# Kernel tuning notes

Measured on AMD Instinct MI355X. Metric: run time of the kernel, lower is better.

The kernel has to match this reference:

```python
import jax, jax.numpy as jnp
import numpy as np
import math

D_SINGLE, D_PAIR, H, PQ, PV = 384, 128, 12, 4, 8
DH = D_SINGLE // H
OUT_DIM = H * DH + H * PV * 4 + H * D_PAIR


def setup_inputs() -> dict:
    key = jax.random.key(0)
    ks = jax.random.split(key, 24)
    B, L = 1, 512
    inp = {
        'single': jax.random.normal(ks[0], (B, L, D_SINGLE), jnp.float32),
        'pair': jax.random.normal(ks[1], (B, L, L, D_PAIR), jnp.float32),
        'rot_mats': jax.random.normal(ks[2], (B, L, 3, 3), jnp.float32),
        'trans': jax.random.normal(ks[3], (B, L, 3), jnp.float32),
        'mask': jnp.ones((B, L), jnp.float32),
        'ln_w': jnp.ones((D_SINGLE,), jnp.float32),
        'ln_b': jnp.zeros((D_SINGLE,), jnp.float32),
        'Wq': jax.random.normal(ks[4], (D_SINGLE, H * DH), jnp.float32) * 0.02,
        'bq': jnp.zeros((H * DH,), jnp.float32),
        'Wk': jax.random.normal(ks[5], (D_SINGLE, H * DH), jnp.float32) * 0.02,
        'bk': jnp.zeros((H * DH,), jnp.float32),
        'Wv': jax.random.normal(ks[6], (D_SINGLE, H * DH), jnp.float32) * 0.02,
        'bv': jnp.zeros((H * DH,), jnp.float32),
        'Wqp': jax.random.normal(ks[7], (D_SINGLE, H * PQ * 3), jnp.float32) * 0.02,
        'bqp': jnp.zeros((H * PQ * 3,), jnp.float32),
        'Wkp': jax.random.normal(ks[8], (D_SINGLE, H * PQ * 3), jnp.float32) * 0.02,
        'bkp': jnp.zeros((H * PQ * 3,), jnp.float32),
        'Wvp': jax.random.normal(ks[9], (D_SINGLE, H * PV * 3), jnp.float32) * 0.02,
        'bvp': jnp.zeros((H * PV * 3,), jnp.float32),
        'Wpb': jax.random.normal(ks[10], (D_PAIR, H), jnp.float32) * 0.02,
        'bpb': jnp.zeros((H,), jnp.float32),
        'Wo': jax.random.normal(ks[11], (OUT_DIM, D_SINGLE), jnp.float32) * 0.02,
        'bo': jnp.zeros((D_SINGLE,), jnp.float32),
        'w_c': jnp.asarray(1.0 / math.sqrt(3.0), jnp.float32),
        'w_l': jnp.asarray(1.0 / 3.0, jnp.float32),
        'gamma_h': jnp.ones((H,), jnp.float32),
    }
    return inp


def _layer_norm(x, w, b, eps=1e-5):
    mu = jnp.mean(x, axis=-1, keepdims=True)
    var = jnp.mean((x - mu) ** 2, axis=-1, keepdims=True)
    return (x - mu) * jax.lax.rsqrt(var + eps) * w + b


def reference(single, pair, rot_mats, trans, mask, ln_w, ln_b, Wq, bq, Wk, bk, Wv, bv,
              Wqp, bqp, Wkp, bkp, Wvp, bvp, Wpb, bpb, Wo, bo, w_c, w_l, gamma_h):
    B, L, _ = single.shape
    sn = _layer_norm(single, ln_w, ln_b)
    q = (sn @ Wq + bq).reshape(B, L, H, DH)
    k = (sn @ Wk + bk).reshape(B, L, H, DH)
    v = (sn @ Wv + bv).reshape(B, L, H, DH)
    qp = (sn @ Wqp + bqp).reshape(B, L, H, PQ, 3)
    kp = (sn @ Wkp + bkp).reshape(B, L, H, PQ, 3)
    vp = (sn @ Wvp + bvp).reshape(B, L, H, PV, 3)

    t = trans[:, :, None, None, :]  # [B,L,1,1,3]
    qg = jnp.einsum('blij,blhpj->blhpi', rot_mats, qp) + t
    kg = jnp.einsum('blij,blhpj->blhpi', rot_mats, kp) + t
    vg = jnp.einsum('blij,blhpj->blhpi', rot_mats, vp) + t

    # sequence logits [B,H,L,L]
    seq_logits = jnp.einsum('bihd,bjhd->bhij', q, k) * w_c / math.sqrt(DH)

    # geometric logits: pairwise point distances [B,H,L,L]
    q_pts = jnp.transpose(qg, (0, 2, 1, 3, 4))  # [B,H,L,PQ,3]
    k_pts = jnp.transpose(kg, (0, 2, 1, 3, 4))
    diff = q_pts[:, :, :, None] - k_pts[:, :, None]  # [B,H,L,L,PQ,3]
    dist_sq = jnp.sum(diff ** 2, axis=-1)            # [B,H,L,L,PQ]
    geo_logits = -0.5 * jnp.sum(dist_sq, axis=-1) * gamma_h[None, :, None, None] * w_l

    pair_bias = jnp.transpose(pair @ Wpb + bpb, (0, 3, 1, 2))  # [B,H,L,L]
    logits = seq_logits + geo_logits + pair_bias

    mask_2d = (mask[:, :, None] * mask[:, None, :])[:, None]  # [B,1,L,L]
    logits = jnp.where(mask_2d > 0, logits, jnp.float32(-1e9))
    attn = jax.nn.softmax(logits, axis=-1)  # [B,H,L,L]

    # sequence aggregation -> [B,L,H,DH]
    seq_out = jnp.einsum('bhij,bjhd->bihd', attn, v).reshape(B, L, H * DH)

    # point aggregation -> local frame features
    pts_out = jnp.einsum('bhij,bjhpd->bihpd', attn, vg)  # [B,L,H,PV,3]
    pts_local = jnp.einsum('blji,blhpj->blhpi', rot_mats, pts_out - t)
    pts_norm = jnp.linalg.norm(pts_local, axis=-1, keepdims=True)
    pts_feat = jnp.concatenate([pts_norm, pts_local], axis=-1).reshape(B, L, H * PV * 4)

    # pair aggregation -> [B,L,H*D_PAIR]
    pair_out = jnp.einsum('bhij,bijd->bihd', attn, pair).reshape(B, L, H * D_PAIR)

    combined = jnp.concatenate([seq_out, pts_feat, pair_out], axis=-1)
    return combined @ Wo + bo
```

## Files before the change

### kernel.cpp

```cpp
#include <hip/hip_runtime.h>
#include <math.h>

#define LQ    512
#define DS    384
#define DPAIR 128
#define NH    12
#define NPP   1792
#define TJC   64
#define NC    8

typedef unsigned short u16;
typedef unsigned int   u32;
typedef __attribute__((ext_vector_type(8))) short bf16x8;
typedef __attribute__((ext_vector_type(4))) float f32x4;

__device__ inline u16 bf16_rne(float x) {
  u32 u = __float_as_uint(x);
  u32 r = (u + 0x7FFFu + ((u >> 16) & 1u)) >> 16;
  return (u16)r;
}
__device__ inline void split_bf16(float x, u16& h, u16& l) {
  u16 hb = bf16_rne(x);
  float hf = __uint_as_float(((u32)hb) << 16);
  h = hb;
  l = bf16_rne(x - hf);
}

__device__ inline void async_copy16(const float* g, float* l) {
  auto gp = (const __attribute__((address_space(1))) float*)(g);
  auto lp = (__attribute__((address_space(3))) float*)(l);
  __builtin_amdgcn_global_load_lds(gp, lp, 16, 0, 0);
}

__global__ __launch_bounds__(256) void k_prep(
    const float* __restrict__ Wq, const float* __restrict__ Wk,
    const float* __restrict__ Wv, const float* __restrict__ Wqp,
    const float* __restrict__ Wkp, const float* __restrict__ Wvp,
    const float* __restrict__ bq, const float* __restrict__ bk,
    const float* __restrict__ bv, const float* __restrict__ bqp,
    const float* __restrict__ bkp, const float* __restrict__ bvp,
    const float* __restrict__ Wpb, const float* __restrict__ Wo,
    const float* __restrict__ xs, const float* __restrict__ ln_w,
    const float* __restrict__ ln_b,
    u16* __restrict__ Wth, u16* __restrict__ Wtl,
    float* __restrict__ bcat, float* __restrict__ WpbT,
    u16* __restrict__ WoTh, u16* __restrict__ WoTl,
    u16* __restrict__ snh, u16* __restrict__ snl) {
  __shared__ u16 sh_hi[64][66], sh_lo[64][66];
  int blk = blockIdx.x, t = threadIdx.x;
  if (blk < 168) {
    int kb = blk / 28, cb = blk % 28;
    int k0 = kb * 64, c0 = cb * 64;
    for (int e = t; e < 4096; e += 256) {
      int rr = e >> 6, cc = e & 63;
      int k = k0 + rr, c = c0 + cc;
      float v = 0.f;
      if (c < 384)       v = Wq[k*384 + c];
      else if (c < 768)  v = Wk[k*384 + c-384];
      else if (c < 1152) v = Wv[k*384 + c-768];
      else if (c < 1296) v = Wqp[k*144 + c-1152];
      else if (c < 1440) v = Wkp[k*144 + c-1296];
      else if (c < 1728) v = Wvp[k*288 + c-1440];
      u16 h_, l_; split_bf16(v, h_, l_);
      sh_hi[rr][cc] = h_; sh_lo[rr][cc] = l_;
    }
    __syncthreads();
    for (int e = t; e < 4096; e += 256) {
      int cc = e >> 6, kk = e & 63;
      Wth[(size_t)(c0+cc)*DS + k0 + kk] = sh_hi[kk][cc];
      Wtl[(size_t)(c0+cc)*DS + k0 + kk] = sh_lo[kk][cc];
    }
  } else if (blk == 168) {
    for (int e = t; e < NPP + NH*DPAIR; e += 256) {
      if (e < NPP) {
        int c = e;
        float v = 0.f;
        if (c < 384)       v = bq[c];
        else if (c < 768)  v = bk[c-384];
        else if (c < 1152) v = bv[c-768];
        else if (c < 1296) v = bqp[c-1152];
        else if (c < 1440) v = bkp[c-1296];
        else if (c < 1728) v = bvp[c-1440];
        bcat[c] = v;
      } else {
        int e2 = e - NPP;
        int k = e2 / NH, h = e2 % NH;
        WpbT[h*DPAIR + k] = Wpb[e2];
      }
    }
  } else if (blk < 385) {
    int idx = blk - 169;
    int kt = idx % 36, nt = idx / 36;
    int k0 = kt * 64, n0 = nt * 64;
    for (int e = t; e < 4096; e += 256) {
      int rr = e >> 6, cc = e & 63;
      float v = Wo[(size_t)(k0+rr)*384 + n0 + cc];
      u16 h_, l_; split_bf16(v, h_, l_);
      sh_hi[rr][cc] = h_; sh_lo[rr][cc] = l_;
    }
    __syncthreads();
    for (int e = t; e < 4096; e += 256) {
      int cc = e >> 6, kk = e & 63;
      WoTh[(size_t)(n0+cc)*2304 + k0 + kk] = sh_hi[kk][cc];
      WoTl[(size_t)(n0+cc)*2304 + k0 + kk] = sh_lo[kk][cc];
    }
  } else {
    int i = blk - 385;
    float* red = (float*)&sh_hi[0][0];
    float a0 = xs[i*DS + t];
    float a1 = (t < 128) ? xs[i*DS + 256 + t] : 0.f;
    red[t] = a0 + a1; __syncthreads();
    for (int s = 128; s > 0; s >>= 1) { if (t < s) red[t] += red[t+s]; __syncthreads(); }
    float mu = red[0] * (1.f/384.f);
    __syncthreads();
    float d0 = a0 - mu, d1 = (t < 128) ? (a1 - mu) : 0.f;
    red[t] = d0*d0 + d1*d1; __syncthreads();
    for (int s = 128; s > 0; s >>= 1) { if (t < s) red[t] += red[t+s]; __syncthreads(); }
    float rstd = rsqrtf(red[0] * (1.f/384.f) + 1e-5f);
    u16 h_, l_;
    float y0 = d0*rstd*ln_w[t] + ln_b[t];
    split_bf16(y0, h_, l_); snh[i*DS + t] = h_; snl[i*DS + t] = l_;
    if (t < 128) {
      float y1 = d1*rstd*ln_w[256+t] + ln_b[256+t];
      split_bf16(y1, h_, l_); snh[i*DS + 256 + t] = h_; snl[i*DS + 256 + t] = l_;
    }
  }
}

__global__ __launch_bounds__(256) void k_gemm_mfma(
    const u16* __restrict__ Ah, const u16* __restrict__ Al,
    const u16* __restrict__ Bth, const u16* __restrict__ Btl,
    const float* __restrict__ bias, float* __restrict__ C,
    float* __restrict__ Cpart, int M, int N, int K) {
  int t = threadIdx.x;
  int lane = t & 63, wave = t >> 6;
  int wr = wave >> 1, wc = wave & 1;
  int i0 = blockIdx.y * 64 + wr * 32;
  int j0 = blockIdx.x * 64 + wc * 32;
  int KS = gridDim.z;
  int kper = K / KS;
  size_t kbeg = (size_t)blockIdx.z * kper;
  int lr = lane & 15, lk = (lane >> 4) << 3;

  const u16* a0h = Ah  + (size_t)(i0 + lr) * K + kbeg + lk;
  const u16* a1h = a0h + (size_t)16 * K;
  const u16* a0l = Al  + (size_t)(i0 + lr) * K + kbeg + lk;
  const u16* a1l = a0l + (size_t)16 * K;
  const u16* b0h = Bth + (size_t)(j0 + lr) * K + kbeg + lk;
  const u16* b1h = b0h + (size_t)16 * K;
  const u16* b0l = Btl + (size_t)(j0 + lr) * K + kbeg + lk;
  const u16* b1l = b0l + (size_t)16 * K;

  f32x4 c00 = {0.f,0.f,0.f,0.f}, c01 = c00, c10 = c00, c11 = c00;
  for (int k = 0; k < kper; k += 32) {
    bf16x8 A0h = *(const bf16x8*)(a0h + k);
    bf16x8 A1h = *(const bf16x8*)(a1h + k);
    bf16x8 B0h = *(const bf16x8*)(b0h + k);
    bf16x8 B1h = *(const bf16x8*)(b1h + k);
    bf16x8 A0l = *(const bf16x8*)(a0l + k);
    bf16x8 A1l = *(const bf16x8*)(a1l + k);
    bf16x8 B0l = *(const bf16x8*)(b0l + k);
    bf16x8 B1l = *(const bf16x8*)(b1l + k);
    c00 = __builtin_amdgcn_mfma_f32_16x16x32_bf16(A0h, B0h, c00, 0, 0, 0);
    c01 = __builtin_amdgcn_mfma_f32_16x16x32_bf16(A0h, B1h, c01, 0, 0, 0);
    c10 = __builtin_amdgcn_mfma_f32_16x16x32_bf16(A1h, B0h, c10, 0, 0, 0);
    c11 = __builtin_amdgcn_mfma_f32_16x16x32_bf16(A1h, B1h, c11, 0, 0, 0);
    c00 = __builtin_amdgcn_mfma_f32_16x16x32_bf16(A0h, B0l, c00, 0, 0, 0);
    c01 = __builtin_amdgcn_mfma_f32_16x16x32_bf16(A0h, B1l, c01, 0, 0, 0);
    c10 = __builtin_amdgcn_mfma_f32_16x16x32_bf16(A1h, B0l, c10, 0, 0, 0);
    c11 = __builtin_amdgcn_mfma_f32_16x16x32_bf16(A1h, B1l, c11, 0, 0, 0);
    c00 = __builtin_amdgcn_mfma_f32_16x16x32_bf16(A0l, B0h, c00, 0, 0, 0);
    c01 = __builtin_amdgcn_mfma_f32_16x16x32_bf16(A0l, B1h, c01, 0, 0, 0);
    c10 = __builtin_amdgcn_mfma_f32_16x16x32_bf16(A1l, B0h, c10, 0, 0, 0);
    c11 = __builtin_amdgcn_mfma_f32_16x16x32_bf16(A1l, B1h, c11, 0, 0, 0);
  }

  int orow = (lane >> 4) << 2;
  int col0 = j0 + lr, col1 = j0 + 16 + lr;
  if (KS == 1) {
    float bb0 = bias[col0], bb1 = bias[col1];
    #pragma unroll
    for (int r = 0; r < 4; r++) {
      int row0 = i0 + orow + r, row1 = row0 + 16;
      C[(size_t)row0*N + col0] = c00[r] + bb0;
      C[(size_t)row0*N + col1] = c01[r] + bb1;
      C[(size_t)row1*N + col0] = c10[r] + bb0;
      C[(size_t)row1*N + col1] = c11[r] + bb1;
    }
  } else {
    float* dst = Cpart + (size_t)blockIdx.z * M * N;
    #pragma unroll
    for (int r = 0; r < 4; r++) {
      int row0 = i0 + orow + r, row1 = row0 + 16;
      dst[(size_t)row0*N + col0] = c00[r];
      dst[(size_t)row0*N + col1] = c01[r];
      dst[(size_t)row1*N + col0] = c10[r];
      dst[(size_t)row1*N + col1] = c11[r];
    }
  }
}

__global__ void k_reduce_bias(const float* __restrict__ part, const float* __restrict__ bias,
                              float* __restrict__ out, int MN, int N, int KS) {
  int e = blockIdx.x * 256 + threadIdx.x;
  if (e >= MN) return;
  float s = bias[e % N];
  for (int z = 0; z < KS; z++) s += part[(size_t)z*MN + e];
  out[e] = s;
}

__global__ __launch_bounds__(256) void k_feat_logits(
    const float* __restrict__ C1, const float* __restrict__ rot,
    const float* __restrict__ trans, const float* __restrict__ gamma,
    const float* __restrict__ w_c, const float* __restrict__ w_l,
    float* __restrict__ S) {
  __shared__ u16 Ash[64][72], Asl[64][72], Bsh[64][72], Bsl[64][72];
  int h = blockIdx.z;
  int i0 = blockIdx.y * 64, j0 = blockIdx.x * 64;
  int t = threadIdx.x;

  if (t < 128) {
    int row = t & 63, side = t >> 6;
    int gi = (side ? j0 : i0) + row;
    float R[9], tr[3];
    #pragma unroll
    for (int r = 0; r < 9; r++) R[r] = rot[(size_t)gi*9 + r];
    #pragma unroll
    for (int r = 0; r < 3; r++) tr[r] = trans[(size_t)gi*3 + r];
    float sc = w_c[0] * rsqrtf(32.f);
    float gp = gamma[h] * w_l[0];
    u16 (*Fh)[72] = side ? Bsh : Ash;
    u16 (*Fl)[72] = side ? Bsl : Asl;
    const float* qk = C1 + (size_t)gi*NPP + (side ? 384 : 0) + h*32;
    u16 h_, l_;
    #pragma unroll 8
    for (int d = 0; d < 32; d++) {
      float v = side ? qk[d] : sc*qk[d];
      split_bf16(v, h_, l_); Fh[row][d] = h_; Fl[row][d] = l_;
    }
    const float* pp = C1 + (size_t)gi*NPP + (side ? 1296 : 1152) + h*12;
    float ss = 0.f;
    #pragma unroll
    for (int p = 0; p < 4; p++) {
      float x = pp[p*3], y = pp[p*3+1], z = pp[p*3+2];
      #pragma unroll
      for (int r = 0; r < 3; r++) {
        float g = fmaf(R[r*3],x, fmaf(R[r*3+1],y, fmaf(R[r*3+2],z, tr[r])));
        float v = side ? g : gp*g;
        split_bf16(v, h_, l_); Fh[row][32+p*3+r] = h_; Fl[row][32+p*3+r] = l_;
        ss = fmaf(g,g,ss);
      }
    }
    float c44 = side ? 1.f : -0.5f*gp*ss;
    float c45 = side ? -0.5f*gp*ss : 1.f;
    split_bf16(c44, h_, l_); Fh[row][44] = h_; Fl[row][44] = l_;
    split_bf16(c45, h_, l_); Fh[row][45] = h_; Fl[row][45] = l_;
    #pragma unroll
    for (int d = 46; d < 64; d++) { Fh[row][d] = 0; Fl[row][d] = 0; }
  }
  __syncthreads();

  int lane = t & 63, wave = t >> 6, wr = wave >> 1, wc = wave & 1;
  int lr = lane & 15, lk = (lane >> 4) << 3;
  f32x4 c00 = {0.f,0.f,0.f,0.f}, c01 = c00, c10 = c00, c11 = c00;
  #pragma unroll
  for (int ks = 0; ks < 64; ks += 32) {
    bf16x8 A0h = *(const bf16x8*)&Ash[wr*32 + lr][ks + lk];
    bf16x8 A1h = *(const bf16x8*)&Ash[wr*32 + 16 + lr][ks + lk];
    bf16x8 B0h = *(const bf16x8*)&Bsh[wc*32 + lr][ks + lk];
    bf16x8 B1h = *(const bf16x8*)&Bsh[wc*32 + 16 + lr][ks + lk];
    bf16x8 A0l = *(const bf16x8*)&Asl[wr*32 + lr][ks + lk];
    bf16x8 A1l = *(const bf16x8*)&Asl[wr*32 + 16 + lr][ks + lk];
    bf16x8 B0l = *(const bf16x8*)&Bsl[wc*32 + lr][ks + lk];
    bf16x8 B1l = *(const bf16x8*)&Bsl[wc*32 + 16 + lr][ks + lk];
    c00 = __builtin_amdgcn_mfma_f32_16x16x32_bf16(A0h, B0h, c00, 0, 0, 0);
    c01 = __builtin_amdgcn_mfma_f32_16x16x32_bf16(A0h, B1h, c01, 0, 0, 0);
    c10 = __builtin_amdgcn_mfma_f32_16x16x32_bf16(A1h, B0h, c10, 0, 0, 0);
    c11 = __builtin_amdgcn_mfma_f32_16x16x32_bf16(A1h, B1h, c11, 0, 0, 0);
    c00 = __builtin_amdgcn_mfma_f32_16x16x32_bf16(A0h, B0l, c00, 0, 0, 0);
    c01 = __builtin_amdgcn_mfma_f32_16x16x32_bf16(A0h, B1l, c01, 0, 0, 0);
    c10 = __builtin_amdgcn_mfma_f32_16x16x32_bf16(A1h, B0l, c10, 0, 0, 0);
    c11 = __builtin_amdgcn_mfma_f32_16x16x32_bf16(A1h, B1l, c11, 0, 0, 0);
    c00 = __builtin_amdgcn_mfma_f32_16x16x32_bf16(A0l, B0h, c00, 0, 0, 0);
    c01 = __builtin_amdgcn_mfma_f32_16x16x32_bf16(A0l, B1h, c01, 0, 0, 0);
    c10 = __builtin_amdgcn_mfma_f32_16x16x32_bf16(A1l, B0h, c10, 0, 0, 0);
    c11 = __builtin_amdgcn_mfma_f32_16x16x32_bf16(A1l, B1h, c11, 0, 0, 0);
  }

  int orow = (lane >> 4) << 2;
  int col0 = j0 + wc*32 + lr, col1 = col0 + 16;
  int rbase = i0 + wr*32 + orow;
  #pragma unroll
  for (int r = 0; r < 4; r++) {
    S[((size_t)h*LQ + rbase + r)*LQ + col0]      = c00[r];
    S[((size_t)h*LQ + rbase + r)*LQ + col1]      = c01[r];
    S[((size_t)h*LQ + rbase + 16 + r)*LQ + col0] = c10[r];
    S[((size_t)h*LQ + rbase + 16 + r)*LQ + col1] = c11[r];
  }
}

__global__ __launch_bounds__(256) void k_vt(
    const float* __restrict__ C1, const float* __restrict__ rot,
    const float* __restrict__ trans,
    u16* __restrict__ Vth, u16* __restrict__ Vtl) {
  int h = blockIdx.x;
  int i = blockIdx.y * 256 + threadIdx.x;
  float R[9], tr[3];
  #pragma unroll
  for (int r = 0; r < 9; r++) R[r] = rot[(size_t)i*9 + r];
  #pragma unroll
  for (int r = 0; r < 3; r++) tr[r] = trans[(size_t)i*3 + r];
  const float* vrow = C1 + (size_t)i*NPP + 768 + h*32;
  const float* prow = C1 + (size_t)i*NPP + 1440 + h*24;
  u16 h_, l_;
  #pragma unroll 8
  for (int n = 0; n < 32; n++) {
    split_bf16(vrow[n], h_, l_);
    Vth[((size_t)h*64 + n)*LQ + i] = h_;
    Vtl[((size_t)h*64 + n)*LQ + i] = l_;
  }
  #pragma unroll
  for (int p = 0; p < 8; p++) {
    float x = prow[p*3], y = prow[p*3+1], z = prow[p*3+2];
    #pragma unroll
    for (int r = 0; r < 3; r++) {
      float g = fmaf(R[r*3],x, fmaf(R[r*3+1],y, fmaf(R[r*3+2],z, tr[r])));
      split_bf16(g, h_, l_);
      Vth[((size_t)h*64 + 32 + p*3 + r)*LQ + i] = h_;
      Vtl[((size_t)h*64 + 32 + p*3 + r)*LQ + i] = l_;
    }
  }
  #pragma unroll
  for (int n = 56; n < 64; n++) {
    Vth[((size_t)h*64 + n)*LQ + i] = 0;
    Vtl[((size_t)h*64 + n)*LQ + i] = 0;
  }
}

__global__ __launch_bounds__(256) void k_pair(
    const float* __restrict__ pair, const float* __restrict__ WpbT,
    const float* __restrict__ bpb, const float* __restrict__ mask,
    float* S, float* __restrict__ scs_g,
    u16* __restrict__ combh, u16* __restrict__ combl) {
  __shared__ float tile[2][TJC*DPAIR];
  __shared__ float wt[NH*TJC];
  __shared__ float msc[NC][NH], ssc[NC][NH];
  __shared__ float rfac[NH], dinv[NH];
  int i = blockIdx.x, t = threadIdx.x;
  int lane = t & 63, wave = t >> 6;
  int j = lane;
  int h0 = wave * 3;
  int dg = t & 31, strip = t >> 5, jb = strip*8;

  const float* prow = pair + (size_t)i*LQ*DPAIR;
  float b0 = bpb[h0], b1 = bpb[h0+1], b2 = bpb[h0+2];
  float mi = mask[i];
  const float* w0p = WpbT + (size_t)(h0+0)*DPAIR;
  const float* w1p = WpbT + (size_t)(h0+1)*DPAIR;
  const float* w2p = WpbT + (size_t)(h0+2)*DPAIR;

  float4 acc[NH];
  #pragma unroll
  for (int h = 0; h < NH; h++) acc[h] = make_float4(0.f,0.f,0.f,0.f);
  float mrun[3] = {-3.0e38f, -3.0e38f, -3.0e38f};

  auto dma = [&](int c, int buf) {
    #pragma unroll
    for (int u = 0; u < 8; u++) {
      int seg = wave*8 + u;
      int F = seg*64 + lane;
      int row = F >> 5, k4s = F & 31;
      int k4 = k4s ^ (row & 7);
      const float* src = prow + (size_t)(c*TJC + row)*DPAIR + k4*4;
      async_copy16(src, &tile[buf][seg*256]);
    }
  };

  dma(0, 0);
  asm volatile("s_waitcnt vmcnt(0)" ::: "memory");
  __syncthreads();
  int cur = 0;

  for (int c = 0; c < NC; c++) {
    if (c < NC-1) dma(c+1, cur^1);
    int j0 = c*TJC;
    float l0 = S[((size_t)(h0+0)*LQ + i)*LQ + j0 + j] + b0;
    float l1 = S[((size_t)(h0+1)*LQ + i)*LQ + j0 + j] + b1;
    float l2 = S[((size_t)(h0+2)*LQ + i)*LQ + j0 + j] + b2;
    {
      float a0 = 0.f, a1 = 0.f, a2 = 0.f;
      #pragma unroll 8
      for (int kk = 0; kk < 32; kk++) {
        float4 pv = *(const float4*)&tile[cur][(j*32 + (kk ^ (j & 7)))*4];
        float4 w0 = *(const float4*)(w0p + kk*4);
        float4 w1 = *(const float4*)(w1p + kk*4);
        float4 w2 = *(const float4*)(w2p + kk*4);
        a0 = fmaf(pv.x,w0.x, fmaf(pv.y,w0.y, fmaf(pv.z,w0.z, fmaf(pv.w,w0.w, a0))));
        a1 = fmaf(pv.x,w1.x, fmaf(pv.y,w1.y, fmaf(pv.z,w1.z, fmaf(pv.w,w1.w, a1))));
        a2 = fmaf(pv.x,w2.x, fmaf(pv.y,w2.y, fmaf(pv.z,w2.z, fmaf(pv.w,w2.w, a2))));
      }
      l0 += a0; l1 += a1; l2 += a2;
      bool dead = (mi * mask[j0 + j] <= 0.f);
      if (dead) { l0 = -1e9f; l1 = -1e9f; l2 = -1e9f; }
    }
    #pragma unroll
    for (int q = 0; q < 3; q++) {
      float lv = (q==0) ? l0 : (q==1) ? l1 : l2;
      float m = lv;
      #pragma unroll
      for (int o = 32; o > 0; o >>= 1) m = fmaxf(m, __shfl_xor(m, o, 64));
      float w = __expf(lv - m);
      float sm = w;
      #pragma unroll
      for (int o = 32; o > 0; o >>= 1) sm += __shfl_xor(sm, o, 64);
      float mnew = fmaxf(mrun[q], m);
      float f  = __expf(m - mnew);
      float rf = __expf(mrun[q] - mnew);
      mrun[q] = mnew;
      wt[(h0+q)*TJC + j] = w * f;
      S[((size_t)(h0+q)*LQ + i)*LQ + j0 + j] = w;
      if (j == 0) { msc[c][h0+q] = m; ssc[c][h0+q] = sm; rfac[h0+q] = rf; }
    }
    __syncthreads();
    {
      float4 pv[8];
      #pragma unroll
      for (int q = 0; q < 8; q++) {
        int row = jb + q;
        pv[q] = *(const float4*)&tile[cur][(row*32 + (dg ^ (row & 7)))*4];
      }
      #pragma unroll
      for (int h = 0; h < NH; h++) {
        float rf = rfac[h];
        float4 w0 = *(const float4*)&wt[h*TJC + jb];
        float4 w1 = *(const float4*)&wt[h*TJC + jb + 4];
        float wq[8] = {w0.x,w0.y,w0.z,w0.w,w1.x,w1.y,w1.z,w1.w};
        float4 a = acc[h];
        a.x *= rf; a.y *= rf; a.z *= rf; a.w *= rf;
        #pragma unroll
        for (int q = 0; q < 8; q++) {
          a.x = fmaf(wq[q], pv[q].x, a.x);
          a.y = fmaf(wq[q], pv[q].y, a.y);
          a.z = fmaf(wq[q], pv[q].z, a.z);
          a.w = fmaf(wq[q], pv[q].w, a.w);
        }
        acc[h] = a;
      }
    }
    asm volatile("s_waitcnt vmcnt(0)" ::: "memory");
    __syncthreads();
    cur ^= 1;
  }

  if (j == 0) {
    #pragma unroll
    for (int q = 0; q < 3; q++) {
      float M = mrun[q];
      float den = 0.f;
      #pragma unroll
      for (int c = 0; c < NC; c++) den += ssc[c][h0+q] * __expf(msc[c][h0+q] - M);
      float inv = 1.f / den;
      dinv[h0+q] = inv;
      #pragma unroll
      for (int c = 0; c < NC; c++)
        scs_g[((size_t)i*NH + h0+q)*NC + c] = __expf(msc[c][h0+q] - M) * inv;
    }
  }

  float4* red4 = (float4*)&tile[0][0];
  float4 tot[2];
  tot[0] = make_float4(0.f,0.f,0.f,0.f);
  tot[1] = make_float4(0.f,0.f,0.f,0.f);
  #pragma unroll
  for (int half = 0; half < 2; half++) {
    if ((strip >> 2) == half) {
      #pragma unroll
      for (int h = 0; h < NH; h++)
        red4[(((strip & 3)*NH) + h)*32 + dg] = acc[h];
    }
    __syncthreads();
    for (int e = t, u = 0; e < NH*32; e += 256, u++) {
      int rh = e >> 5, rd = e & 31;
      #pragma unroll
      for (int s4 = 0; s4 < 4; s4++) {
        float4 v = red4[((s4*NH) + rh)*32 + rd];
        tot[u].x += v.x; tot[u].y += v.y; tot[u].z += v.z; tot[u].w += v.w;
      }
    }
    __syncthreads();
  }
  for (int e = t, u = 0; e < NH*32; e += 256, u++) {
    int rh = e >> 5, rd = e & 31;
    float inv = dinv[rh];
    size_t dst = (size_t)i*2304 + 768 + rh*DPAIR + rd*4;
    u16 h_, l_;
    split_bf16(tot[u].x * inv, h_, l_); combh[dst+0] = h_; combl[dst+0] = l_;
    split_bf16(tot[u].y * inv, h_, l_); combh[dst+1] = h_; combl[dst+1] = l_;
    split_bf16(tot[u].z * inv, h_, l_); combh[dst+2] = h_; combl[dst+2] = l_;
    split_bf16(tot[u].w * inv, h_, l_); combh[dst+3] = h_; combl[dst+3] = l_;
  }
}

__global__ __launch_bounds__(256) void k_attn_mfma(
    const float* __restrict__ S, const float* __restrict__ scs_g,
    const u16* __restrict__ Vth, const u16* __restrict__ Vtl,
    float* __restrict__ psum) {
  int t = threadIdx.x;
  int lane = t & 63, wave = t >> 6;
  int wr = wave >> 1, wc = wave & 1;
  int z = blockIdx.x;
  int i0 = blockIdx.y * 64 + wr * 32;
  int h = blockIdx.z;
  int n0 = wc * 32;
  int lr = lane & 15, lk = (lane >> 4) << 3;

  const float* a0p = S + ((size_t)h*LQ + i0 + lr)*LQ + z*128 + lk;
  const float* a1p = a0p + (size_t)16*LQ;
  const float* s0p = scs_g + ((size_t)(i0 + lr)*NH + h)*NC + z*2;
  const float* s1p = scs_g + ((size_t)(i0 + 16 + lr)*NH + h)*NC + z*2;
  const u16* b0h = Vth + ((size_t)h*64 + n0 + lr)*LQ + z*128 + lk;
  const u16* b1h = b0h + (size_t)16*LQ;
  const u16* b0l = Vtl + ((size_t)h*64 + n0 + lr)*LQ + z*128 + lk;
  const u16* b1l = b0l + (size_t)16*LQ;

  f32x4 c00 = {0.f,0.f,0.f,0.f}, c01 = c00, c10 = c00, c11 = c00;
  #pragma unroll
  for (int k = 0; k < 128; k += 32) {
    int cc = (k >= 64) ? 1 : 0;
    float sc0 = s0p[cc], sc1 = s1p[cc];
    float4 av00 = *(const float4*)(a0p + k);
    float4 av01 = *(const float4*)(a0p + k + 4);
    float4 av10 = *(const float4*)(a1p + k);
    float4 av11 = *(const float4*)(a1p + k + 4);
    float a0v[8] = {av00.x,av00.y,av00.z,av00.w,av01.x,av01.y,av01.z,av01.w};
    float a1v[8] = {av10.x,av10.y,av10.z,av10.w,av11.x,av11.y,av11.z,av11.w};
    bf16x8 A0h = {}, A0l = {}, A1h = {}, A1l = {};
    #pragma unroll
    for (int e = 0; e < 8; e++) {
      u16 hh, ll;
      split_bf16(a0v[e]*sc0, hh, ll);
      A0h[e] = (short)hh; A0l[e] = (short)ll;
      split_bf16(a1v[e]*sc1, hh, ll);
      A1h[e] = (short)hh; A1l[e] = (short)ll;
    }
    bf16x8 B0h = *(const bf16x8*)(b0h + k);
    bf16x8 B1h = *(const bf16x8*)(b1h + k);
    bf16x8 B0l = *(const bf16x8*)(b0l + k);
    bf16x8 B1l = *(const bf16x8*)(b1l + k);
    c00 = __builtin_amdgcn_mfma_f32_16x16x32_bf16(A0h, B0h, c00, 0, 0, 0);
    c01 = __builtin_amdgcn_mfma_f32_16x16x32_bf16(A0h, B1h, c01, 0, 0, 0);
    c10 = __builtin_amdgcn_mfma_f32_16x16x32_bf16(A1h, B0h, c10, 0, 0, 0);
    c11 = __builtin_amdgcn_mfma_f32_16x16x32_bf16(A1h, B1h, c11, 0, 0, 0);
    c00 = __builtin_amdgcn_mfma_f32_16x16x32_bf16(A0h, B0l, c00, 0, 0, 0);
    c01 = __builtin_amdgcn_mfma_f32_16x16x32_bf16(A0h, B1l, c01, 0, 0, 0);
    c10 = __builtin_amdgcn_mfma_f32_16x16x32_bf16(A1h, B0l, c10, 0, 0, 0);
    c11 = __builtin_amdgcn_mfma_f32_16x16x32_bf16(A1h, B1l, c11, 0, 0, 0);
    c00 = __builtin_amdgcn_mfma_f32_16x16x32_bf16(A0l, B0h, c00, 0, 0, 0);
    c01 = __builtin_amdgcn_mfma_f32_16x16x32_bf16(A0l, B1h, c01, 0, 0, 0);
    c10 = __builtin_amdgcn_mfma_f32_16x16x32_bf16(A1l, B0h, c10, 0, 0, 0);
    c11 = __builtin_amdgcn_mfma_f32_16x16x32_bf16(A1l, B1h, c11, 0, 0, 0);
  }

  int orow = (lane >> 4) << 2;
  int col0 = n0 + lr, col1 = n0 + 16 + lr;
  #pragma unroll
  for (int r = 0; r < 4; r++) {
    int row0 = i0 + orow + r, row1 = row0 + 16;
    psum[(((size_t)z*LQ + row0)*NH + h)*64 + col0] = c00[r];
    psum[(((size_t)z*LQ + row0)*NH + h)*64 + col1] = c01[r];
    psum[(((size_t)z*LQ + row1)*NH + h)*64 + col0] = c10[r];
    psum[(((size_t)z*LQ + row1)*NH + h)*64 + col1] = c11[r];
  }
}

__global__ void k_avpts(const float* __restrict__ psum, const float* __restrict__ rot,
                        const float* __restrict__ trans,
                        u16* __restrict__ combh, u16* __restrict__ combl) {
  int idx = blockIdx.x * 256 + threadIdx.x;
  if (idx >= LQ*NH*40) return;
  int w = idx % 40; int ih = idx / 40; int h = ih % NH; int i = ih / NH;
  size_t base = ((size_t)i*NH + h)*64;
  u16 h_, l_;
  if (w < 32) {
    float s = 0.f;
    for (int z = 0; z < 4; z++) s += psum[(size_t)z*LQ*NH*64 + base + w];
    split_bf16(s, h_, l_);
    combh[(size_t)i*2304 + h*32 + w] = h_;
    combl[(size_t)i*2304 + h*32 + w] = l_;
  } else {
    int p = w - 32;
    float g[3];
    #pragma unroll
    for (int r = 0; r < 3; r++) {
      int n = 32 + p*3 + r;
      float s = 0.f;
      for (int z = 0; z < 4; z++) s += psum[(size_t)z*LQ*NH*64 + base + n];
      g[r] = s;
    }
    const float* R = rot + (size_t)i*9;
    const float* tr = trans + (size_t)i*3;
    float x = g[0]-tr[0], y = g[1]-tr[1], z = g[2]-tr[2];
    float lx = fmaf(R[0],x, fmaf(R[3],y, R[6]*z));
    float ly = fmaf(R[1],x, fmaf(R[4],y, R[7]*z));
    float lz = fmaf(R[2],x, fmaf(R[5],y, R[8]*z));
    float nrm = sqrtf(fmaf(lx,lx, fmaf(ly,ly, lz*lz)));
    size_t dst = (size_t)i*2304 + 384 + (h*8 + p)*4;
    split_bf16(nrm, h_, l_); combh[dst+0] = h_; combl[dst+0] = l_;
    split_bf16(lx,  h_, l_); combh[dst+1] = h_; combl[dst+1] = l_;
    split_bf16(ly,  h_, l_); combh[dst+2] = h_; combl[dst+2] = l_;
    split_bf16(lz,  h_, l_); combh[dst+3] = h_; combl[dst+3] = l_;
  }
}

extern "C" void kernel_launch(void* const* d_in, const int* in_sizes, int n_in,
                              void* d_out, int out_size, void* d_ws, size_t ws_size,
                              hipStream_t stream) {
  const float* single = (const float*)d_in[0];
  const float* pair   = (const float*)d_in[1];
  const float* rot    = (const float*)d_in[2];
  const float* trans  = (const float*)d_in[3];
  const float* mask   = (const float*)d_in[4];
  const float* ln_w   = (const float*)d_in[5];
  const float* ln_b   = (const float*)d_in[6];
  const float* Wq     = (const float*)d_in[7];
  const float* bq     = (const float*)d_in[8];
  const float* Wk     = (const float*)d_in[9];
  const float* bk     = (const float*)d_in[10];
  const float* Wv     = (const float*)d_in[11];
  const float* bv     = (const float*)d_in[12];
  const float* Wqp    = (const float*)d_in[13];
  const float* bqp    = (const float*)d_in[14];
  const float* Wkp    = (const float*)d_in[15];
  const float* bkp    = (const float*)d_in[16];
  const float* Wvp    = (const float*)d_in[17];
  const float* bvp    = (const float*)d_in[18];
  const float* Wpb    = (const float*)d_in[19];
  const float* bpb    = (const float*)d_in[20];
  const float* Wo     = (const float*)d_in[21];
  const float* bo     = (const float*)d_in[22];
  const float* w_c    = (const float*)d_in[23];
  const float* w_l    = (const float*)d_in[24];
  const float* gamma  = (const float*)d_in[25];
  float* out = (float*)d_out;

  float* p = (float*)d_ws;
  auto alloc = [&](size_t n) { float* r = p; p += n; return r; };
  u16* WcatTh = (u16*)alloc((size_t)NPP*DS/2);
  u16* WcatTl = (u16*)alloc((size_t)NPP*DS/2);
  u16* snh    = (u16*)alloc((size_t)LQ*DS/2);
  u16* snl    = (u16*)alloc((size_t)LQ*DS/2);
  u16* WoTh   = (u16*)alloc((size_t)DS*2304/2);
  u16* WoTl   = (u16*)alloc((size_t)DS*2304/2);
  u16* combh  = (u16*)alloc((size_t)LQ*2304/2);
  u16* combl  = (u16*)alloc((size_t)LQ*2304/2);
  u16* Vth    = (u16*)alloc((size_t)NH*64*LQ/2);
  u16* Vtl    = (u16*)alloc((size_t)NH*64*LQ/2);
  float* bcat    = alloc(NPP);
  float* WpbT    = alloc((size_t)NH*DPAIR);
  float* C1      = alloc((size_t)LQ*NPP);
  float* S       = alloc((size_t)NH*LQ*LQ);
  float* scs_g   = alloc((size_t)LQ*NH*NC);
  float* psum    = alloc((size_t)4*LQ*NH*64);
  float* outpart = alloc((size_t)8*LQ*DS);

  k_prep<<<dim3(897), 256, 0, stream>>>(
      Wq, Wk, Wv, Wqp, Wkp, Wvp, bq, bk, bv, bqp, bkp, bvp, Wpb, Wo,
      single, ln_w, ln_b, WcatTh, WcatTl, bcat, WpbT, WoTh, WoTl, snh, snl);
  k_gemm_mfma<<<dim3(NPP/64, LQ/64, 1), 256, 0, stream>>>(
      snh, snl, WcatTh, WcatTl, bcat, C1, nullptr, LQ, NPP, DS);
  k_feat_logits<<<dim3(LQ/64, LQ/64, NH), 256, 0, stream>>>(
      C1, rot, trans, gamma, w_c, w_l, S);
  k_vt<<<dim3(NH, LQ/256), 256, 0, stream>>>(C1, rot, trans, Vth, Vtl);
  k_pair<<<dim3(LQ), 256, 0, stream>>>(
      pair, WpbT, bpb, mask, S, scs_g, combh, combl);
  k_attn_mfma<<<dim3(4, LQ/64, NH), 256, 0, stream>>>(
      S, scs_g, Vth, Vtl, psum);
  k_avpts<<<dim3((LQ*NH*40 + 255)/256), 256, 0, stream>>>(
      psum, rot, trans, combh, combl);
  k_gemm_mfma<<<dim3(DS/64, LQ/64, 8), 256, 0, stream>>>(
      combh, combl, WoTh, WoTl, nullptr, nullptr, outpart, LQ, DS, 2304);
  k_reduce_bias<<<dim3((LQ*DS + 255)/256), 256, 0, stream>>>(outpart, bo, out, LQ*DS, DS, 8);
}
```

Measured before the change: 376.1 us.

## Split pair-attention kernel into per-chunk blocks with separate softmax combine kernel

The per-row pair kernel, which looped serially over 8 key chunks with async double-buffered loads and an online softmax, is replaced by a grid of (row, chunk) blocks. Each block computes local softmax stats and a partial pair aggregation into a global workspace, and a new small kernel merges the chunk maxima and sums and writes the normalized pair output. This gives 8x more blocks for the pass over the large pair tensor and drops the serial dependency, at the cost of a partial-sum round trip through global memory, an extra launch, and plain (non-async) tile loads.

```diff
diff --git a/kernel.cpp b/kernel.cpp
--- a/kernel.cpp
+++ b/kernel.cpp
@@ -24,12 +24,6 @@
   float hf = __uint_as_float(((u32)hb) << 16);
   h = hb;
   l = bf16_rne(x - hf);
-}
-
-__device__ inline void async_copy16(const float* g, float* l) {
-  auto gp = (const __attribute__((address_space(1))) float*)(g);
-  auto lp = (__attribute__((address_space(3))) float*)(l);
-  __builtin_amdgcn_global_load_lds(gp, lp, 16, 0, 0);
 }
 
 __global__ __launch_bounds__(256) void k_prep(
@@ -337,137 +331,94 @@
   }
 }
 
-__global__ __launch_bounds__(256) void k_pair(
+__global__ __launch_bounds__(256, 2) void k_pair_chunk(
     const float* __restrict__ pair, const float* __restrict__ WpbT,
     const float* __restrict__ bpb, const float* __restrict__ mask,
-    float* S, float* __restrict__ scs_g,
-    u16* __restrict__ combh, u16* __restrict__ combl) {
-  __shared__ float tile[2][TJC*DPAIR];
+    float* __restrict__ S, float* __restrict__ pairpart, float* __restrict__ msum) {
+  __shared__ float tile[TJC*133];
   __shared__ float wt[NH*TJC];
-  __shared__ float msc[NC][NH], ssc[NC][NH];
-  __shared__ float rfac[NH], dinv[NH];
-  int i = blockIdx.x, t = threadIdx.x;
-  int lane = t & 63, wave = t >> 6;
-  int j = lane;
-  int h0 = wave * 3;
+  int i = blockIdx.x, c = blockIdx.y, t = threadIdx.x;
+  int j0 = c*TJC;
+
+  const float4* src = (const float4*)(pair + ((size_t)i*LQ + j0)*DPAIR);
+  #pragma unroll
+  for (int u = 0; u < 8; u++) {
+    int e = t + u*256; int row = e >> 5, c4 = e & 31;
+    *(float4*)&tile[row*133 + c4*4] = src[e];
+  }
+
+  int j = t & 63;
+  int hg = __builtin_amdgcn_readfirstlane(t >> 6);
+  int h0 = hg*3;
+  float l[3];
+  #pragma unroll
+  for (int q = 0; q < 3; q++)
+    l[q] = S[((size_t)(h0+q)*LQ + i)*LQ + j0 + j] + bpb[h0+q];
+  bool dead = (mask[i] * mask[j0 + j] <= 0.f);
+  __syncthreads();
+
+  {
+    const float* w0p = WpbT + (size_t)(h0+0)*DPAIR;
+    const float* w1p = WpbT + (size_t)(h0+1)*DPAIR;
+    const float* w2p = WpbT + (size_t)(h0+2)*DPAIR;
+    float a0 = 0.f, a1 = 0.f, a2 = 0.f;
+    #pragma unroll 8
+    for (int k = 0; k < DPAIR; k += 4) {
+      float4 pv = *(const float4*)&tile[j*133 + k];
+      float4 w0 = *(const float4*)(w0p + k);
+      float4 w1 = *(const float4*)(w1p + k);
+      float4 w2 = *(const float4*)(w2p + k);
+      a0 = fmaf(pv.x,w0.x, fmaf(pv.y,w0.y, fmaf(pv.z,w0.z, fmaf(pv.w,w0.w, a0))));
+      a1 = fmaf(pv.x,w1.x, fmaf(pv.y,w1.y, fmaf(pv.z,w1.z, fmaf(pv.w,w1.w, a1))));
+      a2 = fmaf(pv.x,w2.x, fmaf(pv.y,w2.y, fmaf(pv.z,w2.z, fmaf(pv.w,w2.w, a2))));
+    }
+    l[0] += a0; l[1] += a1; l[2] += a2;
+    if (dead) { l[0] = -1e9f; l[1] = -1e9f; l[2] = -1e9f; }
+  }
+
+  #pragma unroll
+  for (int q = 0; q < 3; q++) {
+    float m = l[q];
+    #pragma unroll
+    for (int o = 32; o > 0; o >>= 1) m = fmaxf(m, __shfl_xor(m, o, 64));
+    float w = __expf(l[q] - m);
+    float sm = w;
+    #pragma unroll
+    for (int o = 32; o > 0; o >>= 1) sm += __shfl_xor(sm, o, 64);
+    wt[(h0+q)*TJC + j] = w;
+    S[((size_t)(h0+q)*LQ + i)*LQ + j0 + j] = w;
+    if (j == 0) {
+      float* dst = msum + (((size_t)i*NC + c)*NH + h0 + q)*2;
+      dst[0] = m; dst[1] = sm;
+    }
+  }
+  __syncthreads();
+
   int dg = t & 31, strip = t >> 5, jb = strip*8;
-
-  const float* prow = pair + (size_t)i*LQ*DPAIR;
-  float b0 = bpb[h0], b1 = bpb[h0+1], b2 = bpb[h0+2];
-  float mi = mask[i];
-  const float* w0p = WpbT + (size_t)(h0+0)*DPAIR;
-  const float* w1p = WpbT + (size_t)(h0+1)*DPAIR;
-  const float* w2p = WpbT + (size_t)(h0+2)*DPAIR;
-
+  float4 pv[8];
+  #pragma unroll
+  for (int q = 0; q < 8; q++) pv[q] = *(const float4*)&tile[(jb+q)*133 + dg*4];
   float4 acc[NH];
   #pragma unroll
   for (int h = 0; h < NH; h++) acc[h] = make_float4(0.f,0.f,0.f,0.f);
-  float mrun[3] = {-3.0e38f, -3.0e38f, -3.0e38f};
-
-  auto dma = [&](int c, int buf) {
-    #pragma unroll
-    for (int u = 0; u < 8; u++) {
-      int seg = wave*8 + u;
-      int F = seg*64 + lane;
-      int row = F >> 5, k4s = F & 31;
-      int k4 = k4s ^ (row & 7);
-      const float* src = prow + (size_t)(c*TJC + row)*DPAIR + k4*4;
-      async_copy16(src, &tile[buf][seg*256]);
-    }
-  };
-
-  dma(0, 0);
-  asm volatile("s_waitcnt vmcnt(0)" ::: "memory");
+  #pragma unroll
+  for (int h = 0; h < NH; h++) {
+    float4 w0 = *(const float4*)&wt[h*TJC + jb];
+    float4 w1 = *(const float4*)&wt[h*TJC + jb + 4];
+    float wq[8] = {w0.x,w0.y,w0.z,w0.w,w1.x,w1.y,w1.z,w1.w};
+    float4 a = acc[h];
+    #pragma unroll
+    for (int q = 0; q < 8; q++) {
+      a.x = fmaf(wq[q], pv[q].x, a.x);
+      a.y = fmaf(wq[q], pv[q].y, a.y);
+      a.z = fmaf(wq[q], pv[q].z, a.z);
+      a.w = fmaf(wq[q], pv[q].w, a.w);
+    }
+    acc[h] = a;
+  }
   __syncthreads();
-  int cur = 0;
-
-  for (int c = 0; c < NC; c++) {
-    if (c < NC-1) dma(c+1, cur^1);
-    int j0 = c*TJC;
-    float l0 = S[((size_t)(h0+0)*LQ + i)*LQ + j0 + j] + b0;
-    float l1 = S[((size_t)(h0+1)*LQ + i)*LQ + j0 + j] + b1;
-    float l2 = S[((size_t)(h0+2)*LQ + i)*LQ + j0 + j] + b2;
-    {
-      float a0 = 0.f, a1 = 0.f, a2 = 0.f;
-      #pragma unroll 8
-      for (int kk = 0; kk < 32; kk++) {
-        float4 pv = *(const float4*)&tile[cur][(j*32 + (kk ^ (j & 7)))*4];
-        float4 w0 = *(const float4*)(w0p + kk*4);
-        float4 w1 = *(const float4*)(w1p + kk*4);
-        float4 w2 = *(const float4*)(w2p + kk*4);
-        a0 = fmaf(pv.x,w0.x, fmaf(pv.y,w0.y, fmaf(pv.z,w0.z, fmaf(pv.w,w0.w, a0))));
-        a1 = fmaf(pv.x,w1.x, fmaf(pv.y,w1.y, fmaf(pv.z,w1.z, fmaf(pv.w,w1.w, a1))));
-        a2 = fmaf(pv.x,w2.x, fmaf(pv.y,w2.y, fmaf(pv.z,w2.z, fmaf(pv.w,w2.w, a2))));
-      }
-      l0 += a0; l1 += a1; l2 += a2;
-      bool dead = (mi * mask[j0 + j] <= 0.f);
-      if (dead) { l0 = -1e9f; l1 = -1e9f; l2 = -1e9f; }
-    }
-    #pragma unroll
-    for (int q = 0; q < 3; q++) {
-      float lv = (q==0) ? l0 : (q==1) ? l1 : l2;
-      float m = lv;
-      #pragma unroll
-      for (int o = 32; o > 0; o >>= 1) m = fmaxf(m, __shfl_xor(m, o, 64));
-      float w = __expf(lv - m);
-      float sm = w;
-      #pragma unroll
-      for (int o = 32; o > 0; o >>= 1) sm += __shfl_xor(sm, o, 64);
-      float mnew = fmaxf(mrun[q], m);
-      float f  = __expf(m - mnew);
-      float rf = __expf(mrun[q] - mnew);
-      mrun[q] = mnew;
-      wt[(h0+q)*TJC + j] = w * f;
-      S[((size_t)(h0+q)*LQ + i)*LQ + j0 + j] = w;
-      if (j == 0) { msc[c][h0+q] = m; ssc[c][h0+q] = sm; rfac[h0+q] = rf; }
-    }
-    __syncthreads();
-    {
-      float4 pv[8];
-      #pragma unroll
-      for (int q = 0; q < 8; q++) {
-        int row = jb + q;
-        pv[q] = *(const float4*)&tile[cur][(row*32 + (dg ^ (row & 7)))*4];
-      }
-      #pragma unroll
-      for (int h = 0; h < NH; h++) {
-        float rf = rfac[h];
-        float4 w0 = *(const float4*)&wt[h*TJC + jb];
-        float4 w1 = *(const float4*)&wt[h*TJC + jb + 4];
-        float wq[8] = {w0.x,w0.y,w0.z,w0.w,w1.x,w1.y,w1.z,w1.w};
-        float4 a = acc[h];
-        a.x *= rf; a.y *= rf; a.z *= rf; a.w *= rf;
-        #pragma unroll
-        for (int q = 0; q < 8; q++) {
-          a.x = fmaf(wq[q], pv[q].x, a.x);
-          a.y = fmaf(wq[q], pv[q].y, a.y);
-          a.z = fmaf(wq[q], pv[q].z, a.z);
-          a.w = fmaf(wq[q], pv[q].w, a.w);
-        }
-        acc[h] = a;
-      }
-    }
-    asm volatile("s_waitcnt vmcnt(0)" ::: "memory");
-    __syncthreads();
-    cur ^= 1;
-  }
-
-  if (j == 0) {
-    #pragma unroll
-    for (int q = 0; q < 3; q++) {
-      float M = mrun[q];
-      float den = 0.f;
-      #pragma unroll
-      for (int c = 0; c < NC; c++) den += ssc[c][h0+q] * __expf(msc[c][h0+q] - M);
-      float inv = 1.f / den;
-      dinv[h0+q] = inv;
-      #pragma unroll
-      for (int c = 0; c < NC; c++)
-        scs_g[((size_t)i*NH + h0+q)*NC + c] = __expf(msc[c][h0+q] - M) * inv;
-    }
-  }
-
-  float4* red4 = (float4*)&tile[0][0];
+
+  float4* red4 = (float4*)tile;
   float4 tot[2];
   tot[0] = make_float4(0.f,0.f,0.f,0.f);
   tot[1] = make_float4(0.f,0.f,0.f,0.f);
@@ -491,14 +442,52 @@
   }
   for (int e = t, u = 0; e < NH*32; e += 256, u++) {
     int rh = e >> 5, rd = e & 31;
-    float inv = dinv[rh];
-    size_t dst = (size_t)i*2304 + 768 + rh*DPAIR + rd*4;
-    u16 h_, l_;
-    split_bf16(tot[u].x * inv, h_, l_); combh[dst+0] = h_; combl[dst+0] = l_;
-    split_bf16(tot[u].y * inv, h_, l_); combh[dst+1] = h_; combl[dst+1] = l_;
-    split_bf16(tot[u].z * inv, h_, l_); combh[dst+2] = h_; combl[dst+2] = l_;
-    split_bf16(tot[u].w * inv, h_, l_); combh[dst+3] = h_; combl[dst+3] = l_;
-  }
+    *(float4*)&pairpart[(((size_t)i*NC + c)*NH + rh)*DPAIR + rd*4] = tot[u];
+  }
+}
+
+__global__ __launch_bounds__(384) void k_scs_pairout(
+    const float* __restrict__ msum, const float* __restrict__ pairpart,
+    float* __restrict__ scs_g,
+    u16* __restrict__ combh, u16* __restrict__ combl) {
+  __shared__ float scs[NH*NC];
+  int i = blockIdx.x, t = threadIdx.x;
+  if (t < NH) {
+    float m = -3.0e38f;
+    float mc[NC], sc_[NC];
+    #pragma unroll
+    for (int c = 0; c < NC; c++) {
+      const float* p = msum + (((size_t)i*NC + c)*NH + t)*2;
+      mc[c] = p[0]; sc_[c] = p[1];
+      m = fmaxf(m, mc[c]);
+    }
+    float s = 0.f;
+    #pragma unroll
+    for (int c = 0; c < NC; c++) s += sc_[c] * __expf(mc[c] - m);
+    float inv = 1.f / s;
+    #pragma unroll
+    for (int c = 0; c < NC; c++) {
+      float v = __expf(mc[c] - m) * inv;
+      scs[t*NC + c] = v;
+      scs_g[((size_t)i*NH + t)*NC + c] = v;
+    }
+  }
+  __syncthreads();
+  int h = t >> 5, d = t & 31;
+  float4 tot = make_float4(0.f,0.f,0.f,0.f);
+  #pragma unroll
+  for (int c = 0; c < NC; c++) {
+    float sc = scs[h*NC + c];
+    float4 v = *(const float4*)&pairpart[(((size_t)i*NC + c)*NH + h)*DPAIR + d*4];
+    tot.x = fmaf(v.x, sc, tot.x); tot.y = fmaf(v.y, sc, tot.y);
+    tot.z = fmaf(v.z, sc, tot.z); tot.w = fmaf(v.w, sc, tot.w);
+  }
+  size_t dst = (size_t)i*2304 + 768 + h*DPAIR + d*4;
+  u16 h_, l_;
+  split_bf16(tot.x, h_, l_); combh[dst+0] = h_; combl[dst+0] = l_;
+  split_bf16(tot.y, h_, l_); combh[dst+1] = h_; combl[dst+1] = l_;
+  split_bf16(tot.z, h_, l_); combh[dst+2] = h_; combl[dst+2] = l_;
+  split_bf16(tot.w, h_, l_); combh[dst+3] = h_; combl[dst+3] = l_;
 }
 
 __global__ __launch_bounds__(256) void k_attn_mfma(
@@ -659,6 +648,8 @@
   float* WpbT    = alloc((size_t)NH*DPAIR);
   float* C1      = alloc((size_t)LQ*NPP);
   float* S       = alloc((size_t)NH*LQ*LQ);
+  float* pairpart= alloc((size_t)LQ*NC*NH*DPAIR);
+  float* msum    = alloc((size_t)LQ*NC*NH*2);
   float* scs_g   = alloc((size_t)LQ*NH*NC);
   float* psum    = alloc((size_t)4*LQ*NH*64);
   float* outpart = alloc((size_t)8*LQ*DS);
@@ -671,8 +662,10 @@
   k_feat_logits<<<dim3(LQ/64, LQ/64, NH), 256, 0, stream>>>(
       C1, rot, trans, gamma, w_c, w_l, S);
   k_vt<<<dim3(NH, LQ/256), 256, 0, stream>>>(C1, rot, trans, Vth, Vtl);
-  k_pair<<<dim3(LQ), 256, 0, stream>>>(
-      pair, WpbT, bpb, mask, S, scs_g, combh, combl);
+  k_pair_chunk<<<dim3(LQ, NC), 256, 0, stream>>>(
+      pair, WpbT, bpb, mask, S, pairpart, msum);
+  k_scs_pairout<<<dim3(LQ), 384, 0, stream>>>(
+      msum, pairpart, scs_g, combh, combl);
   k_attn_mfma<<<dim3(4, LQ/64, NH), 256, 0, stream>>>(
       S, scs_g, Vth, Vtl, psum);
   k_avpts<<<dim3((LQ*NH*40 + 255)/256), 256, 0, stream>>>(
```

Result: faster. 347.2 us (-7.7%).
